# Kernel optimization log

Measured on AMD Instinct MI355X. Metric: run time of the kernel, lower is better.

Reference implementation:

```python
import jax, jax.numpy as jnp
import numpy as np

PROMPT_LEN = 2048
VOCAB = 49408
DIM = 768


def setup_inputs() -> dict:
    key = jax.random.key(0)
    k1, k2 = jax.random.split(key)
    # prompt_embs initialized ~ N(0, 0.02) per nn.init.normal_(std=0.02)
    prompt_embs = jax.random.normal(k1, (PROMPT_LEN, DIM), dtype=jnp.float32) * 0.02
    # codebook (CLIP embedding table), fixed data (not a trainable param)
    clip_embs = jax.random.normal(k2, (VOCAB, DIM), dtype=jnp.float32)
    return {"prompt_embs": prompt_embs, "clip_embs": clip_embs}


def _find_nearest(prompt_embs, clip_embs):
    # torch.cdist with p=2 -> Euclidean distance. argmin is invariant under sqrt,
    # so we use the expanded squared-distance form (single GEMM + norms),
    # avoiding materializing the [P, D]-broadcast difference tensor.
    p_sq = jnp.sum(prompt_embs * prompt_embs, axis=-1, keepdims=True)  # [P, 1]
    c_sq = jnp.sum(clip_embs * clip_embs, axis=-1)                      # [V]
    cross = jnp.einsum("pd,vd->pv", prompt_embs, clip_embs)            # [P, V]
    d2 = p_sq + c_sq[None, :] - 2.0 * cross                             # [P, V]
    return jnp.argmin(d2, axis=1)                                       # [P]


def reference(prompt_embs, clip_embs):
    prompt_ids = _find_nearest(prompt_embs, clip_embs)      # [P] int
    vocab_embs = clip_embs[prompt_ids, :]                   # [P, D] gather
    # straight-through: value = vocab_embs, gradient flows to prompt_embs
    out_embs = jax.lax.stop_gradient(vocab_embs - prompt_embs) + prompt_embs
    return out_embs, prompt_ids
```

## Files before the change

### kernel.cpp

```cpp
#include <hip/hip_runtime.h>
#include <float.h>

#define PROMPT_LEN 2048
#define VOCAB 49408
#define DIM 768
#define ROWS_TOTAL (VOCAB + PROMPT_LEN)
#define NS 32
#define BM 64
#define BN 64
#define KCH 128
#define NCHUNK (DIM / KCH)
#define LDK (KCH + 8)
#define CAND_MAX 4096
#define EPS 0.008f

typedef __attribute__((ext_vector_type(8))) short s8v;
typedef __attribute__((ext_vector_type(4))) float fx4;


__device__ inline unsigned short f2bf(float x) {
    unsigned u = __float_as_uint(x);
    u += 0x7FFFu + ((u >> 16) & 1u);
    return (unsigned short)(u >> 16);
}

__device__ inline void merge2(float& b1, float& b2, int& bi,
                              float y1, float y2, int yi) {
    if (y1 < b1) { b2 = fminf(b1, y2); b1 = y1; bi = yi; }
    else         { b2 = fminf(b2, fminf(y1, y2)); }
}

__global__ void __launch_bounds__(1024) k_sumsq(const float* __restrict__ prompt,
                                                const float* __restrict__ clip,
                                                float* __restrict__ csq,
                                                unsigned* __restrict__ scal) {
    int tid  = threadIdx.x;
    int wid  = tid >> 6;
    int lane = tid & 63;
    int base = blockIdx.x * 128 + wid * 8;

    if (blockIdx.x == 0 && tid == 0) scal[0] = 0u;

    float locMin = FLT_MAX, locMax = 0.f;
    for (int r = base; r < base + 8; r += 2) {
        const float* s0 = (r     < VOCAB) ? clip + (size_t)r * DIM
                                          : prompt + (size_t)(r - VOCAB) * DIM;
        const float* s1 = (r + 1 < VOCAB) ? clip + (size_t)(r + 1) * DIM
                                          : prompt + (size_t)(r + 1 - VOCAB) * DIM;
        float4 a0 = ((const float4*)s0)[lane];
        float4 a1 = ((const float4*)s0)[64 + lane];
        float4 a2 = ((const float4*)s0)[128 + lane];
        float4 b0 = ((const float4*)s1)[lane];
        float4 b1 = ((const float4*)s1)[64 + lane];
        float4 b2 = ((const float4*)s1)[128 + lane];
        float sA = a0.x*a0.x + a0.y*a0.y + a0.z*a0.z + a0.w*a0.w
                 + a1.x*a1.x + a1.y*a1.y + a1.z*a1.z + a1.w*a1.w
                 + a2.x*a2.x + a2.y*a2.y + a2.z*a2.z + a2.w*a2.w;
        float sB = b0.x*b0.x + b0.y*b0.y + b0.z*b0.z + b0.w*b0.w
                 + b1.x*b1.x + b1.y*b1.y + b1.z*b1.z + b1.w*b1.w
                 + b2.x*b2.x + b2.y*b2.y + b2.z*b2.z + b2.w*b2.w;
        #pragma unroll
        for (int m = 32; m >= 1; m >>= 1) {
            sA += __shfl_xor(sA, m, 64);
            sB += __shfl_xor(sB, m, 64);
        }
        if (r < VOCAB)     locMin = fminf(locMin, sA); else locMax = fmaxf(locMax, sA);
        if (r + 1 < VOCAB) locMin = fminf(locMin, sB); else locMax = fmaxf(locMax, sB);
        if (lane == 0) {
            if (r < VOCAB)     csq[r] = sA;
            if (r + 1 < VOCAB) csq[r + 1] = sB;
        }
    }
    __shared__ float smn[16], smx[16];
    if (lane == 0) { smn[wid] = locMin; smx[wid] = locMax; }
    __syncthreads();
    if (tid == 0) {
        float mn = FLT_MAX, mx = 0.f;
        #pragma unroll
        for (int w = 0; w < 16; ++w) { mn = fminf(mn, smn[w]); mx = fmaxf(mx, smx[w]); }
        atomicMin(&scal[1], __float_as_uint(mn));
        atomicMax((int*)&scal[2], (int)__float_as_uint(mx));
    }
}

__global__ void __launch_bounds__(256) k_compact(const float* __restrict__ csq,
                                                 int* __restrict__ cand,
                                                 unsigned* __restrict__ scal) {
    float cmin    = __uint_as_float(scal[1]);
    float pmax_sq = __uint_as_float(scal[2]);
    float B  = sqrtf(pmax_sq) * 1.0001f + 1e-6f;
    float U  = cmin + 2.f * B * sqrtf(cmin) + 1.0f;
    float sT = B + sqrtf(B * B + U);
    float T  = sT * sT;
    int v = blockIdx.x * 256 + threadIdx.x;
    if (v == 0) scal[3] = 0u;
    __shared__ int cnt, basep;
    if (threadIdx.x == 0) cnt = 0;
    __syncthreads();
    int keep = (v < VOCAB) && (csq[v] <= T);
    int pos = 0;
    if (keep) pos = atomicAdd(&cnt, 1);
    __syncthreads();
    if (threadIdx.x == 0 && cnt > 0) basep = atomicAdd((int*)&scal[0], cnt);
    __syncthreads();
    if (keep) cand[basep + pos] = v;
}

__global__ void __launch_bounds__(256) k_convert(const float* __restrict__ prompt,
                                                 const float* __restrict__ clip,
                                                 const int* __restrict__ cand,
                                                 const unsigned* __restrict__ scal,
                                                 unsigned short* __restrict__ PbH,
                                                 unsigned short* __restrict__ PbL,
                                                 unsigned short* __restrict__ CbH,
                                                 unsigned short* __restrict__ CbL) {
    int count = (int)scal[0];
    if (count > CAND_MAX) count = CAND_MAX;
    int rows = PROMPT_LEN + count;
    int wid  = threadIdx.x >> 6;
    int lane = threadIdx.x & 63;
    for (int r = blockIdx.x * 4 + wid; r < rows; r += gridDim.x * 4) {
        const float* src;
        unsigned short *dH, *dL;
        if (r < PROMPT_LEN) {
            src = prompt + (size_t)r * DIM;
            dH = PbH + (size_t)r * DIM;  dL = PbL + (size_t)r * DIM;
        } else {
            int i = r - PROMPT_LEN;
            src = clip + (size_t)cand[i] * DIM;
            dH = CbH + (size_t)i * DIM;  dL = CbL + (size_t)i * DIM;
        }
        #pragma unroll
        for (int i = 0; i < 3; ++i) {
            float4 x = ((const float4*)src)[i * 64 + lane];
            ushort4 h, l;
            h.x = f2bf(x.x); l.x = f2bf(x.x - __uint_as_float((unsigned)h.x << 16));
            h.y = f2bf(x.y); l.y = f2bf(x.y - __uint_as_float((unsigned)h.y << 16));
            h.z = f2bf(x.z); l.z = f2bf(x.z - __uint_as_float((unsigned)h.z << 16));
            h.w = f2bf(x.w); l.w = f2bf(x.w - __uint_as_float((unsigned)h.w << 16));
            ((ushort4*)dH)[i * 64 + lane] = h;
            ((ushort4*)dL)[i * 64 + lane] = l;
        }
    }
}

__global__ void __launch_bounds__(256, 2)
k_score(const unsigned short* __restrict__ PbH, const unsigned short* __restrict__ PbL,
        const unsigned short* __restrict__ CbH, const unsigned short* __restrict__ CbL,
        const float* __restrict__ csq, const int* __restrict__ cand,
        const unsigned* __restrict__ scal,
        float* __restrict__ AB1, float* __restrict__ AB2, int* __restrict__ AIdx) {
    int mi = blockIdx.x & 31;
    int s  = blockIdx.x >> 5;
    int m0 = mi * BM;
    int count = (int)scal[0];
    if (count > CAND_MAX) count = CAND_MAX;
    int ntiles = (count + BN - 1) / BN;

    int tid  = threadIdx.x;
    int lane = tid & 63;
    int wid  = tid >> 6;
    int wr32 = (wid >> 1) * 32;
    int wc32 = (wid & 1) * 32;
    int l15  = lane & 15;
    int l4   = lane >> 4;

    __shared__ unsigned short Ah[BM][LDK], Al[BM][LDK];
    __shared__ unsigned short Bh[BN][LDK], Bl[BN][LDK];
    __shared__ int   candS[BN];
    __shared__ float csqS[BN];
    __shared__ float mB1[BM][2], mB2[BM][2];
    __shared__ int   mBI[BM][2];

    int srow[4], scol[4], offA[4];
    #pragma unroll
    for (int f = 0; f < 4; ++f) {
        int j = tid + 256 * f;
        srow[f] = j >> 4;
        scol[f] = (j & 15) * 8;
        offA[f] = (m0 + srow[f]) * DIM + scol[f];
    }

    float rb1[2][4], rb2[2][4]; int rbi[2][4];
    #pragma unroll
    for (int fm = 0; fm < 2; ++fm)
        #pragma unroll
        for (int j = 0; j < 4; ++j) { rb1[fm][j] = FLT_MAX; rb2[fm][j] = FLT_MAX; rbi[fm][j] = 0x7fffffff; }

    for (int tile = s; tile < ntiles; tile += NS) {
        __syncthreads();
        if (tid < BN) {
            int ci = tile * BN + tid;
            int v  = (ci < count) ? cand[ci] : 0;
            candS[tid] = v;
            csqS[tid]  = (ci < count) ? csq[v] : FLT_MAX;
        }

        int offB[4];
        #pragma unroll
        for (int f = 0; f < 4; ++f) {
            int rowc = tile * BN + srow[f];
            if (rowc >= count) rowc = 0;
            offB[f] = rowc * DIM + scol[f];
        }

        fx4 acc00 = {0.f,0.f,0.f,0.f}, acc01 = {0.f,0.f,0.f,0.f};
        fx4 acc10 = {0.f,0.f,0.f,0.f}, acc11 = {0.f,0.f,0.f,0.f};

        s8v rAh[4], rAl[4], rBh[4], rBl[4];
        #pragma unroll
        for (int f = 0; f < 4; ++f) {
            rAh[f] = *(const s8v*)(PbH + offA[f]);
            rAl[f] = *(const s8v*)(PbL + offA[f]);
            rBh[f] = *(const s8v*)(CbH + offB[f]);
            rBl[f] = *(const s8v*)(CbL + offB[f]);
        }

        #pragma unroll
        for (int kc = 0; kc < NCHUNK; ++kc) {
            __syncthreads();
            #pragma unroll
            for (int f = 0; f < 4; ++f) {
                *(s8v*)&Ah[srow[f]][scol[f]] = rAh[f];
                *(s8v*)&Al[srow[f]][scol[f]] = rAl[f];
                *(s8v*)&Bh[srow[f]][scol[f]] = rBh[f];
                *(s8v*)&Bl[srow[f]][scol[f]] = rBl[f];
            }
            __syncthreads();
            if (kc + 1 < NCHUNK) {
                int off = (kc + 1) * KCH;
                #pragma unroll
                for (int f = 0; f < 4; ++f) {
                    rAh[f] = *(const s8v*)(PbH + offA[f] + off);
                    rAl[f] = *(const s8v*)(PbL + offA[f] + off);
                    rBh[f] = *(const s8v*)(CbH + offB[f] + off);
                    rBl[f] = *(const s8v*)(CbL + offB[f] + off);
                }
            }
            #pragma unroll
            for (int kk = 0; kk < KCH / 32; ++kk) {
                int ko = kk * 32 + l4 * 8;
                s8v ah0 = *(const s8v*)&Ah[wr32      + l15][ko];
                s8v ah1 = *(const s8v*)&Ah[wr32 + 16 + l15][ko];
                s8v al0 = *(const s8v*)&Al[wr32      + l15][ko];
                s8v al1 = *(const s8v*)&Al[wr32 + 16 + l15][ko];
                s8v bh0 = *(const s8v*)&Bh[wc32      + l15][ko];
                s8v bh1 = *(const s8v*)&Bh[wc32 + 16 + l15][ko];
                s8v bl0 = *(const s8v*)&Bl[wc32      + l15][ko];
                s8v bl1 = *(const s8v*)&Bl[wc32 + 16 + l15][ko];
                acc00 = __builtin_amdgcn_mfma_f32_16x16x32_bf16(ah0, bh0, acc00, 0, 0, 0);
                acc01 = __builtin_amdgcn_mfma_f32_16x16x32_bf16(ah0, bh1, acc01, 0, 0, 0);
                acc10 = __builtin_amdgcn_mfma_f32_16x16x32_bf16(ah1, bh0, acc10, 0, 0, 0);
                acc11 = __builtin_amdgcn_mfma_f32_16x16x32_bf16(ah1, bh1, acc11, 0, 0, 0);
                acc00 = __builtin_amdgcn_mfma_f32_16x16x32_bf16(al0, bh0, acc00, 0, 0, 0);
                acc01 = __builtin_amdgcn_mfma_f32_16x16x32_bf16(al0, bh1, acc01, 0, 0, 0);
                acc10 = __builtin_amdgcn_mfma_f32_16x16x32_bf16(al1, bh0, acc10, 0, 0, 0);
                acc11 = __builtin_amdgcn_mfma_f32_16x16x32_bf16(al1, bh1, acc11, 0, 0, 0);
                acc00 = __builtin_amdgcn_mfma_f32_16x16x32_bf16(ah0, bl0, acc00, 0, 0, 0);
                acc01 = __builtin_amdgcn_mfma_f32_16x16x32_bf16(ah0, bl1, acc01, 0, 0, 0);
                acc10 = __builtin_amdgcn_mfma_f32_16x16x32_bf16(ah1, bl0, acc10, 0, 0, 0);
                acc11 = __builtin_amdgcn_mfma_f32_16x16x32_bf16(ah1, bl1, acc11, 0, 0, 0);
            }
        }

        float cs0 = csqS[wc32 + l15];       int v0 = candS[wc32 + l15];
        float cs1 = csqS[wc32 + 16 + l15];  int v1 = candS[wc32 + 16 + l15];
        #pragma unroll
        for (int j = 0; j < 4; ++j) {
            if (cs0 < FLT_MAX) {
                float d2 = fmaf(-2.f, acc00[j], cs0);
                if (d2 < rb1[0][j]) { rb2[0][j] = rb1[0][j]; rb1[0][j] = d2; rbi[0][j] = v0; }
                else if (d2 <= rb2[0][j]) rb2[0][j] = d2;
                d2 = fmaf(-2.f, acc10[j], cs0);
                if (d2 < rb1[1][j]) { rb2[1][j] = rb1[1][j]; rb1[1][j] = d2; rbi[1][j] = v0; }
                else if (d2 <= rb2[1][j]) rb2[1][j] = d2;
            }
            if (cs1 < FLT_MAX) {
                float d2 = fmaf(-2.f, acc01[j], cs1);
                if (d2 < rb1[0][j]) { rb2[0][j] = rb1[0][j]; rb1[0][j] = d2; rbi[0][j] = v1; }
                else if (d2 <= rb2[0][j]) rb2[0][j] = d2;
                d2 = fmaf(-2.f, acc11[j], cs1);
                if (d2 < rb1[1][j]) { rb2[1][j] = rb1[1][j]; rb1[1][j] = d2; rbi[1][j] = v1; }
                else if (d2 <= rb2[1][j]) rb2[1][j] = d2;
            }
        }
    }

    #pragma unroll
    for (int fm = 0; fm < 2; ++fm)
        #pragma unroll
        for (int j = 0; j < 4; ++j) {
            float b1 = rb1[fm][j], b2 = rb2[fm][j]; int bi = rbi[fm][j];
            #pragma unroll
            for (int msk = 1; msk <= 8; msk <<= 1) {
                float y1 = __shfl_xor(b1, msk, 64);
                float y2 = __shfl_xor(b2, msk, 64);
                int   yi = __shfl_xor(bi, msk, 64);
                merge2(b1, b2, bi, y1, y2, yi);
            }
            if (l15 == 0) {
                int rl = wr32 + fm * 16 + l4 * 4 + j;
                int wc = (wid & 1);
                mB1[rl][wc] = b1; mB2[rl][wc] = b2; mBI[rl][wc] = bi;
            }
        }
    __syncthreads();
    if (tid < BM) {
        float B1 = mB1[tid][0], B2 = mB2[tid][0]; int BI = mBI[tid][0];
        merge2(B1, B2, BI, mB1[tid][1], mB2[tid][1], mBI[tid][1]);
        int m = m0 + tid;
        AB1[m * NS + s]  = B1;
        AB2[m * NS + s]  = B2;
        AIdx[m * NS + s] = BI;
    }
}

__global__ void __launch_bounds__(256) k_merge(const float* __restrict__ prompt,
                                               const float* __restrict__ clip,
                                               const float* __restrict__ AB1,
                                               const float* __restrict__ AB2,
                                               const int* __restrict__ AIdx,
                                               unsigned* __restrict__ scal,
                                               int* __restrict__ amb,
                                               float* __restrict__ out) {
    int wid  = threadIdx.x >> 6;
    int lane = threadIdx.x & 63;
    int m = blockIdx.x * 4 + wid;
    int s = lane & 31;
    int count = (int)scal[0];

    float b1 = AB1[m * NS + s];
    float b2 = AB2[m * NS + s];
    int   bi = AIdx[m * NS + s];
    #pragma unroll
    for (int msk = 1; msk <= 16; msk <<= 1) {
        float y1 = __shfl_xor(b1, msk, 64);
        float y2 = __shfl_xor(b2, msk, 64);
        int   yi = __shfl_xor(bi, msk, 64);
        merge2(b1, b2, bi, y1, y2, yi);
    }

    if (count > CAND_MAX || b2 - b1 < EPS) {
        if (lane == 0) {
            int pos = atomicAdd((int*)&scal[3], 1);
            amb[pos] = m;
        }
    } else {
        const float* crow = clip + (size_t)bi * DIM;
        const float* prow = prompt + (size_t)m * DIM;
        #pragma unroll
        for (int i = 0; i < 3; ++i) {
            float4 c = ((const float4*)crow)[i * 64 + lane];
            float4 p = ((const float4*)prow)[i * 64 + lane];
            float4 o;
            o.x = (c.x - p.x) + p.x;
            o.y = (c.y - p.y) + p.y;
            o.z = (c.z - p.z) + p.z;
            o.w = (c.w - p.w) + p.w;
            ((float4*)(out + (size_t)m * DIM))[i * 64 + lane] = o;
        }
        if (lane == 0) out[(size_t)PROMPT_LEN * DIM + m] = (float)bi;
    }
}

__global__ void __launch_bounds__(1024) k_fallback(const float* __restrict__ prompt,
                                                   const float* __restrict__ clip,
                                                   const int* __restrict__ cand,
                                                   const unsigned* __restrict__ scal,
                                                   const int* __restrict__ amb,
                                                   float* __restrict__ out) {
    int nAmb  = (int)scal[3];
    int count = (int)scal[0];
    int tid  = threadIdx.x;
    int wid  = tid >> 6;
    int lane = tid & 63;

    __shared__ double fB[16];
    __shared__ int    fI[16];
    __shared__ int    sWin;

    for (int a = blockIdx.x; a < nAmb; a += gridDim.x) {
        int m = amb[a];
        const float* prow = prompt + (size_t)m * DIM;
        double pd[12];
        #pragma unroll
        for (int i = 0; i < 3; ++i) {
            float4 v = ((const float4*)prow)[i * 64 + lane];
            pd[i*4+0] = (double)v.x; pd[i*4+1] = (double)v.y;
            pd[i*4+2] = (double)v.z; pd[i*4+3] = (double)v.w;
        }
        double best = 1e300;
        int bestIdx = 0x7fffffff;
        for (int ci = wid; ci < count; ci += 16) {
            int v = cand[ci];
            const float* crow = clip + (size_t)v * DIM;
            double sd = 0.0;
            #pragma unroll
            for (int i = 0; i < 3; ++i) {
                float4 c = ((const float4*)crow)[i * 64 + lane];
                double d0 = (double)c.x - pd[i*4+0];
                double d1 = (double)c.y - pd[i*4+1];
                double d2 = (double)c.z - pd[i*4+2];
                double d3 = (double)c.w - pd[i*4+3];
                sd = fma(d0, d0, sd); sd = fma(d1, d1, sd);
                sd = fma(d2, d2, sd); sd = fma(d3, d3, sd);
            }
            #pragma unroll
            for (int msk = 32; msk >= 1; msk >>= 1) sd += __shfl_xor(sd, msk, 64);
            if (sd < best || (sd == best && v < bestIdx)) { best = sd; bestIdx = v; }
        }
        if (lane == 0) { fB[wid] = best; fI[wid] = bestIdx; }
        __syncthreads();
        if (tid == 0) {
            double b = fB[0]; int bi2 = fI[0];
            #pragma unroll
            for (int w = 1; w < 16; ++w)
                if (fB[w] < b || (fB[w] == b && fI[w] < bi2)) { b = fB[w]; bi2 = fI[w]; }
            sWin = bi2;
        }
        __syncthreads();
        int win = sWin;

        if (tid < 192) {
            float4 c = ((const float4*)(clip + (size_t)win * DIM))[tid];
            float4 p = ((const float4*)prow)[tid];
            float4 o;
            o.x = (c.x - p.x) + p.x;
            o.y = (c.y - p.y) + p.y;
            o.z = (c.z - p.z) + p.z;
            o.w = (c.w - p.w) + p.w;
            ((float4*)(out + (size_t)m * DIM))[tid] = o;
        }
        if (tid == 0) out[(size_t)PROMPT_LEN * DIM + m] = (float)win;
        __syncthreads();
    }
}

extern "C" void kernel_launch(void* const* d_in, const int* in_sizes, int n_in,
                              void* d_out, int out_size, void* d_ws, size_t ws_size,
                              hipStream_t stream) {
    const float* prompt = (const float*)d_in[0];
    const float* clip   = (const float*)d_in[1];
    float* out = (float*)d_out;

    char* w = (char*)d_ws;
    float*    csq  = (float*)w;                    w += (size_t)VOCAB * 4;
    int*      cand = (int*)w;                      w += (size_t)VOCAB * 4;
    unsigned* scal = (unsigned*)w;                 w += 32;
    float*    AB1  = (float*)w;                    w += (size_t)PROMPT_LEN * NS * 4;
    float*    AB2  = (float*)w;                    w += (size_t)PROMPT_LEN * NS * 4;
    int*      AIdx = (int*)w;                      w += (size_t)PROMPT_LEN * NS * 4;
    int*      amb  = (int*)w;                      w += (size_t)PROMPT_LEN * 4;
    unsigned short* PbH = (unsigned short*)w;      w += (size_t)PROMPT_LEN * DIM * 2;
    unsigned short* PbL = (unsigned short*)w;      w += (size_t)PROMPT_LEN * DIM * 2;
    unsigned short* CbH = (unsigned short*)w;      w += (size_t)CAND_MAX * DIM * 2;
    unsigned short* CbL = (unsigned short*)w;      w += (size_t)CAND_MAX * DIM * 2;

    k_sumsq<<<ROWS_TOTAL / 128, 1024, 0, stream>>>(prompt, clip, csq, scal);
    k_compact<<<(VOCAB + 255) / 256, 256, 0, stream>>>(csq, cand, scal);
    k_convert<<<1024, 256, 0, stream>>>(prompt, clip, cand, scal, PbH, PbL, CbH, CbL);
    k_score<<<32 * NS, 256, 0, stream>>>(PbH, PbL, CbH, CbL, csq, cand, scal,
                                         AB1, AB2, AIdx);
    k_merge<<<PROMPT_LEN / 4, 256, 0, stream>>>(prompt, clip, AB1, AB2, AIdx, scal, amb, out);
    k_fallback<<<128, 1024, 0, stream>>>(prompt, clip, cand, scal, amb, out);
}
```

Before: 307.8 us.

## Fuse compact with convert and merge into score via last-block reduction

Merges the candidate-compaction and bf16 split conversion into a single kernel, folds the per-row argmin merge and output write into the score kernel using an atomic counter so the last split block per row tile does the reduction, and cuts the K-split count from 32 to 8. It also caches candidate norms contiguously and uses smaller sumsq blocks. The goal is to remove two launches and the intermediate round trips. In exchange it adds atomic and fence synchronisation, and because each score block now handles more tiles there may be less parallelism in the GEMM stage.

```diff
diff --git a/kernel.cpp b/kernel.cpp
--- a/kernel.cpp
+++ b/kernel.cpp
@@ -5,7 +5,8 @@
 #define VOCAB 49408
 #define DIM 768
 #define ROWS_TOTAL (VOCAB + PROMPT_LEN)
-#define NS 32
+#define NS 8
+#define NMI (PROMPT_LEN / 64)
 #define BM 64
 #define BN 64
 #define KCH 128
@@ -30,14 +31,30 @@
     else         { b2 = fminf(b2, fminf(y1, y2)); }
 }
 
-__global__ void __launch_bounds__(1024) k_sumsq(const float* __restrict__ prompt,
-                                                const float* __restrict__ clip,
-                                                float* __restrict__ csq,
-                                                unsigned* __restrict__ scal) {
+__device__ inline void conv_row(const float* __restrict__ src,
+                                unsigned short* __restrict__ dH,
+                                unsigned short* __restrict__ dL, int lane) {
+    #pragma unroll
+    for (int i = 0; i < 3; ++i) {
+        float4 x = ((const float4*)src)[i * 64 + lane];
+        ushort4 h, l;
+        h.x = f2bf(x.x); l.x = f2bf(x.x - __uint_as_float((unsigned)h.x << 16));
+        h.y = f2bf(x.y); l.y = f2bf(x.y - __uint_as_float((unsigned)h.y << 16));
+        h.z = f2bf(x.z); l.z = f2bf(x.z - __uint_as_float((unsigned)h.z << 16));
+        h.w = f2bf(x.w); l.w = f2bf(x.w - __uint_as_float((unsigned)h.w << 16));
+        ((ushort4*)dH)[i * 64 + lane] = h;
+        ((ushort4*)dL)[i * 64 + lane] = l;
+    }
+}
+
+__global__ void __launch_bounds__(256) k_sumsq(const float* __restrict__ prompt,
+                                               const float* __restrict__ clip,
+                                               float* __restrict__ csq,
+                                               unsigned* __restrict__ scal) {
     int tid  = threadIdx.x;
     int wid  = tid >> 6;
     int lane = tid & 63;
-    int base = blockIdx.x * 128 + wid * 8;
+    int base = blockIdx.x * 32 + wid * 8;
 
     if (blockIdx.x == 0 && tid == 0) scal[0] = 0u;
 
@@ -71,90 +88,87 @@
             if (r + 1 < VOCAB) csq[r + 1] = sB;
         }
     }
-    __shared__ float smn[16], smx[16];
+    __shared__ float smn[4], smx[4];
     if (lane == 0) { smn[wid] = locMin; smx[wid] = locMax; }
     __syncthreads();
     if (tid == 0) {
         float mn = FLT_MAX, mx = 0.f;
         #pragma unroll
-        for (int w = 0; w < 16; ++w) { mn = fminf(mn, smn[w]); mx = fmaxf(mx, smx[w]); }
+        for (int w = 0; w < 4; ++w) { mn = fminf(mn, smn[w]); mx = fmaxf(mx, smx[w]); }
         atomicMin(&scal[1], __float_as_uint(mn));
         atomicMax((int*)&scal[2], (int)__float_as_uint(mx));
     }
 }
 
-__global__ void __launch_bounds__(256) k_compact(const float* __restrict__ csq,
-                                                 int* __restrict__ cand,
-                                                 unsigned* __restrict__ scal) {
+__global__ void __launch_bounds__(256) k_compact_convert(
+        const float* __restrict__ prompt, const float* __restrict__ clip,
+        const float* __restrict__ csq,
+        int* __restrict__ cand, float* __restrict__ candCsq,
+        unsigned* __restrict__ scal, int* __restrict__ cnt,
+        unsigned short* __restrict__ PbH, unsigned short* __restrict__ PbL,
+        unsigned short* __restrict__ CbH, unsigned short* __restrict__ CbL) {
     float cmin    = __uint_as_float(scal[1]);
     float pmax_sq = __uint_as_float(scal[2]);
     float B  = sqrtf(pmax_sq) * 1.0001f + 1e-6f;
     float U  = cmin + 2.f * B * sqrtf(cmin) + 1.0f;
     float sT = B + sqrtf(B * B + U);
     float T  = sT * sT;
-    int v = blockIdx.x * 256 + threadIdx.x;
-    if (v == 0) scal[3] = 0u;
-    __shared__ int cnt, basep;
-    if (threadIdx.x == 0) cnt = 0;
-    __syncthreads();
-    int keep = (v < VOCAB) && (csq[v] <= T);
+
+    int tid = threadIdx.x;
+    int v   = blockIdx.x * 256 + tid;
+    if (blockIdx.x == 0) {
+        if (tid == 0) scal[3] = 0u;
+        if (tid < NMI) cnt[tid] = 0;
+    }
+    __shared__ int cntS, basep;
+    __shared__ int kvS[256];
+    if (tid == 0) cntS = 0;
+    __syncthreads();
+    float cs = csq[v];
+    int keep = (cs <= T);
     int pos = 0;
-    if (keep) pos = atomicAdd(&cnt, 1);
-    __syncthreads();
-    if (threadIdx.x == 0 && cnt > 0) basep = atomicAdd((int*)&scal[0], cnt);
-    __syncthreads();
-    if (keep) cand[basep + pos] = v;
-}
-
-__global__ void __launch_bounds__(256) k_convert(const float* __restrict__ prompt,
-                                                 const float* __restrict__ clip,
-                                                 const int* __restrict__ cand,
-                                                 const unsigned* __restrict__ scal,
-                                                 unsigned short* __restrict__ PbH,
-                                                 unsigned short* __restrict__ PbL,
-                                                 unsigned short* __restrict__ CbH,
-                                                 unsigned short* __restrict__ CbL) {
-    int count = (int)scal[0];
-    if (count > CAND_MAX) count = CAND_MAX;
-    int rows = PROMPT_LEN + count;
-    int wid  = threadIdx.x >> 6;
-    int lane = threadIdx.x & 63;
-    for (int r = blockIdx.x * 4 + wid; r < rows; r += gridDim.x * 4) {
-        const float* src;
-        unsigned short *dH, *dL;
-        if (r < PROMPT_LEN) {
-            src = prompt + (size_t)r * DIM;
-            dH = PbH + (size_t)r * DIM;  dL = PbL + (size_t)r * DIM;
-        } else {
-            int i = r - PROMPT_LEN;
-            src = clip + (size_t)cand[i] * DIM;
-            dH = CbH + (size_t)i * DIM;  dL = CbL + (size_t)i * DIM;
-        }
-        #pragma unroll
-        for (int i = 0; i < 3; ++i) {
-            float4 x = ((const float4*)src)[i * 64 + lane];
-            ushort4 h, l;
-            h.x = f2bf(x.x); l.x = f2bf(x.x - __uint_as_float((unsigned)h.x << 16));
-            h.y = f2bf(x.y); l.y = f2bf(x.y - __uint_as_float((unsigned)h.y << 16));
-            h.z = f2bf(x.z); l.z = f2bf(x.z - __uint_as_float((unsigned)h.z << 16));
-            h.w = f2bf(x.w); l.w = f2bf(x.w - __uint_as_float((unsigned)h.w << 16));
-            ((ushort4*)dH)[i * 64 + lane] = h;
-            ((ushort4*)dL)[i * 64 + lane] = l;
-        }
+    if (keep) pos = atomicAdd(&cntS, 1);
+    __syncthreads();
+    if (tid == 0 && cntS > 0) basep = atomicAdd((int*)&scal[0], cntS);
+    __syncthreads();
+    if (keep) {
+        cand[basep + pos]    = v;
+        candCsq[basep + pos] = cs;
+        kvS[pos] = v;
+    }
+    __syncthreads();
+
+    int nk   = cntS;
+    int wid  = tid >> 6;
+    int lane = tid & 63;
+    for (int i = wid; i < nk; i += 4) {
+        int dst = basep + i;
+        if (dst >= CAND_MAX) break;
+        conv_row(clip + (size_t)kvS[i] * DIM,
+                 CbH + (size_t)dst * DIM, CbL + (size_t)dst * DIM, lane);
+    }
+    #pragma unroll
+    for (int j = wid; j < 11; j += 4) {
+        int r = blockIdx.x + 193 * j;
+        if (r < PROMPT_LEN)
+            conv_row(prompt + (size_t)r * DIM,
+                     PbH + (size_t)r * DIM, PbL + (size_t)r * DIM, lane);
     }
 }
 
 __global__ void __launch_bounds__(256, 2)
 k_score(const unsigned short* __restrict__ PbH, const unsigned short* __restrict__ PbL,
         const unsigned short* __restrict__ CbH, const unsigned short* __restrict__ CbL,
-        const float* __restrict__ csq, const int* __restrict__ cand,
-        const unsigned* __restrict__ scal,
-        float* __restrict__ AB1, float* __restrict__ AB2, int* __restrict__ AIdx) {
-    int mi = blockIdx.x & 31;
+        const float* __restrict__ candCsq, const int* __restrict__ cand,
+        unsigned* __restrict__ scal, int* __restrict__ cnt,
+        float* __restrict__ AB1, float* __restrict__ AB2, int* __restrict__ AIdx,
+        const float* __restrict__ prompt, const float* __restrict__ clip,
+        int* __restrict__ amb, float* __restrict__ out) {
+    int mi = blockIdx.x & (NMI - 1);
     int s  = blockIdx.x >> 5;
     int m0 = mi * BM;
-    int count = (int)scal[0];
-    if (count > CAND_MAX) count = CAND_MAX;
+    int rawCount = (int)scal[0];
+    int count = rawCount > CAND_MAX ? CAND_MAX : rawCount;
     int ntiles = (count + BN - 1) / BN;
 
     int tid  = threadIdx.x;
@@ -169,8 +183,10 @@
     __shared__ unsigned short Bh[BN][LDK], Bl[BN][LDK];
     __shared__ int   candS[BN];
     __shared__ float csqS[BN];
-    __shared__ float mB1[BM][2], mB2[BM][2];
-    __shared__ int   mBI[BM][2];
+    __shared__ float mB1[BM][4], mB2[BM][4];
+    __shared__ int   mBI[BM][4];
+    __shared__ int   winS[BM], clearS[BM];
+    __shared__ int   lastS;
 
     int srow[4], scol[4], offA[4];
     #pragma unroll
@@ -191,9 +207,8 @@
         __syncthreads();
         if (tid < BN) {
             int ci = tile * BN + tid;
-            int v  = (ci < count) ? cand[ci] : 0;
-            candS[tid] = v;
-            csqS[tid]  = (ci < count) ? csq[v] : FLT_MAX;
+            candS[tid] = (ci < count) ? cand[ci] : 0;
+            csqS[tid]  = (ci < count) ? candCsq[ci] : FLT_MAX;
         }
 
         int offB[4];
@@ -300,8 +315,7 @@
             }
             if (l15 == 0) {
                 int rl = wr32 + fm * 16 + l4 * 4 + j;
-                int wc = (wid & 1);
-                mB1[rl][wc] = b1; mB2[rl][wc] = b2; mBI[rl][wc] = bi;
+                mB1[rl][wid & 1] = b1; mB2[rl][wid & 1] = b2; mBI[rl][wid & 1] = bi;
             }
         }
     __syncthreads();
@@ -309,45 +323,53 @@
         float B1 = mB1[tid][0], B2 = mB2[tid][0]; int BI = mBI[tid][0];
         merge2(B1, B2, BI, mB1[tid][1], mB2[tid][1], mBI[tid][1]);
         int m = m0 + tid;
-        AB1[m * NS + s]  = B1;
-        AB2[m * NS + s]  = B2;
-        AIdx[m * NS + s] = BI;
-    }
-}
-
-__global__ void __launch_bounds__(256) k_merge(const float* __restrict__ prompt,
-                                               const float* __restrict__ clip,
-                                               const float* __restrict__ AB1,
-                                               const float* __restrict__ AB2,
-                                               const int* __restrict__ AIdx,
-                                               unsigned* __restrict__ scal,
-                                               int* __restrict__ amb,
-                                               float* __restrict__ out) {
-    int wid  = threadIdx.x >> 6;
-    int lane = threadIdx.x & 63;
-    int m = blockIdx.x * 4 + wid;
-    int s = lane & 31;
-    int count = (int)scal[0];
-
-    float b1 = AB1[m * NS + s];
-    float b2 = AB2[m * NS + s];
-    int   bi = AIdx[m * NS + s];
-    #pragma unroll
-    for (int msk = 1; msk <= 16; msk <<= 1) {
-        float y1 = __shfl_xor(b1, msk, 64);
-        float y2 = __shfl_xor(b2, msk, 64);
-        int   yi = __shfl_xor(bi, msk, 64);
-        merge2(b1, b2, bi, y1, y2, yi);
-    }
-
-    if (count > CAND_MAX || b2 - b1 < EPS) {
-        if (lane == 0) {
+        __hip_atomic_store(&AB1[m * NS + s], B1, __ATOMIC_RELAXED, __HIP_MEMORY_SCOPE_AGENT);
+        __hip_atomic_store(&AB2[m * NS + s], B2, __ATOMIC_RELAXED, __HIP_MEMORY_SCOPE_AGENT);
+        __hip_atomic_store(&AIdx[m * NS + s], BI, __ATOMIC_RELAXED, __HIP_MEMORY_SCOPE_AGENT);
+    }
+    __syncthreads();
+    if (tid == 0) {
+        __threadfence();
+        int old = atomicAdd(&cnt[mi], 1);
+        lastS = (old == NS - 1);
+    }
+    __syncthreads();
+    if (!lastS) return;
+    __threadfence();
+
+    {
+        int r = tid & 63, g = tid >> 6;
+        int m = m0 + r;
+        float b1 = FLT_MAX, b2 = FLT_MAX; int bi = 0x7fffffff;
+        #pragma unroll
+        for (int ss = 0; ss < 2; ++ss) {
+            int s2 = g * 2 + ss;
+            float y1 = __hip_atomic_load(&AB1[m * NS + s2], __ATOMIC_RELAXED, __HIP_MEMORY_SCOPE_AGENT);
+            float y2 = __hip_atomic_load(&AB2[m * NS + s2], __ATOMIC_RELAXED, __HIP_MEMORY_SCOPE_AGENT);
+            int   yi = __hip_atomic_load(&AIdx[m * NS + s2], __ATOMIC_RELAXED, __HIP_MEMORY_SCOPE_AGENT);
+            merge2(b1, b2, bi, y1, y2, yi);
+        }
+        mB1[r][g] = b1; mB2[r][g] = b2; mBI[r][g] = bi;
+    }
+    __syncthreads();
+    if (tid < BM) {
+        float B1 = mB1[tid][0], B2 = mB2[tid][0]; int BI = mBI[tid][0];
+        #pragma unroll
+        for (int gg = 1; gg < 4; ++gg)
+            merge2(B1, B2, BI, mB1[tid][gg], mB2[tid][gg], mBI[tid][gg]);
+        int clear = (rawCount <= CAND_MAX) && (B2 - B1 >= EPS);
+        winS[tid] = BI; clearS[tid] = clear;
+        if (!clear) {
             int pos = atomicAdd((int*)&scal[3], 1);
-            amb[pos] = m;
-        }
-    } else {
-        const float* crow = clip + (size_t)bi * DIM;
-        const float* prow = prompt + (size_t)m * DIM;
+            amb[pos] = m0 + tid;
+        }
+    }
+    __syncthreads();
+    for (int rr = wid; rr < BM; rr += 4) {
+        if (!clearS[rr]) continue;
+        int mm = m0 + rr, win = winS[rr];
+        const float* crow = clip + (size_t)win * DIM;
+        const float* prow = prompt + (size_t)mm * DIM;
         #pragma unroll
         for (int i = 0; i < 3; ++i) {
             float4 c = ((const float4*)crow)[i * 64 + lane];
@@ -357,9 +379,9 @@
             o.y = (c.y - p.y) + p.y;
             o.z = (c.z - p.z) + p.z;
             o.w = (c.w - p.w) + p.w;
-            ((float4*)(out + (size_t)m * DIM))[i * 64 + lane] = o;
-        }
-        if (lane == 0) out[(size_t)PROMPT_LEN * DIM + m] = (float)bi;
+            ((float4*)(out + (size_t)mm * DIM))[i * 64 + lane] = o;
+        }
+        if (lane == 0) out[(size_t)PROMPT_LEN * DIM + mm] = (float)win;
     }
 }
 
@@ -444,23 +466,24 @@
     float* out = (float*)d_out;
 
     char* w = (char*)d_ws;
-    float*    csq  = (float*)w;                    w += (size_t)VOCAB * 4;
-    int*      cand = (int*)w;                      w += (size_t)VOCAB * 4;
-    unsigned* scal = (unsigned*)w;                 w += 32;
-    float*    AB1  = (float*)w;                    w += (size_t)PROMPT_LEN * NS * 4;
-    float*    AB2  = (float*)w;                    w += (size_t)PROMPT_LEN * NS * 4;
-    int*      AIdx = (int*)w;                      w += (size_t)PROMPT_LEN * NS * 4;
-    int*      amb  = (int*)w;                      w += (size_t)PROMPT_LEN * 4;
+    float*    csq     = (float*)w;                 w += (size_t)VOCAB * 4;
+    int*      cand    = (int*)w;                   w += (size_t)VOCAB * 4;
+    float*    candCsq = (float*)w;                 w += (size_t)VOCAB * 4;
+    unsigned* scal    = (unsigned*)w;              w += 32;
+    float*    AB1     = (float*)w;                 w += (size_t)PROMPT_LEN * NS * 4;
+    float*    AB2     = (float*)w;                 w += (size_t)PROMPT_LEN * NS * 4;
+    int*      AIdx    = (int*)w;                   w += (size_t)PROMPT_LEN * NS * 4;
+    int*      amb     = (int*)w;                   w += (size_t)PROMPT_LEN * 4;
+    int*      cnt     = (int*)w;                   w += 128;
     unsigned short* PbH = (unsigned short*)w;      w += (size_t)PROMPT_LEN * DIM * 2;
     unsigned short* PbL = (unsigned short*)w;      w += (size_t)PROMPT_LEN * DIM * 2;
     unsigned short* CbH = (unsigned short*)w;      w += (size_t)CAND_MAX * DIM * 2;
     unsigned short* CbL = (unsigned short*)w;      w += (size_t)CAND_MAX * DIM * 2;
 
-    k_sumsq<<<ROWS_TOTAL / 128, 1024, 0, stream>>>(prompt, clip, csq, scal);
-    k_compact<<<(VOCAB + 255) / 256, 256, 0, stream>>>(csq, cand, scal);
-    k_convert<<<1024, 256, 0, stream>>>(prompt, clip, cand, scal, PbH, PbL, CbH, CbL);
-    k_score<<<32 * NS, 256, 0, stream>>>(PbH, PbL, CbH, CbL, csq, cand, scal,
-                                         AB1, AB2, AIdx);
-    k_merge<<<PROMPT_LEN / 4, 256, 0, stream>>>(prompt, clip, AB1, AB2, AIdx, scal, amb, out);
+    k_sumsq<<<ROWS_TOTAL / 32, 256, 0, stream>>>(prompt, clip, csq, scal);
+    k_compact_convert<<<VOCAB / 256, 256, 0, stream>>>(prompt, clip, csq, cand, candCsq,
+                                                       scal, cnt, PbH, PbL, CbH, CbL);
+    k_score<<<NMI * NS, 256, 0, stream>>>(PbH, PbL, CbH, CbL, candCsq, cand, scal, cnt,
+                                          AB1, AB2, AIdx, prompt, clip, amb, out);
     k_fallback<<<128, 1024, 0, stream>>>(prompt, clip, cand, scal, amb, out);
 }
```

New measurement: 332.8 us. +8.1%, slower.

## Fuse candidate compaction with bf16 conversion and shrink sumsq grid

Applied to the files above, without the earlier changes.

Merges the compaction and bf16 hi/lo conversion kernels into one. Each block compacts its slice of vocab rows and converts its kept candidate rows, while also converting four prompt rows. This removes one launch and the separate pass that re-read the candidate list. It also stores candidate squared norms contiguously so the scoring kernel avoids an indirect csq lookup, and it changes the sumsq kernel to a grid-stride loop over 512 blocks. The block-local conversion puts a different amount of work on each block, so load balance depends on how candidates are distributed.

```diff
diff --git a/kernel.cpp b/kernel.cpp
--- a/kernel.cpp
+++ b/kernel.cpp
@@ -24,6 +24,22 @@
     return (unsigned short)(u >> 16);
 }
 
+__device__ inline void conv_row(const float* __restrict__ src,
+                                unsigned short* __restrict__ dH,
+                                unsigned short* __restrict__ dL, int lane) {
+    #pragma unroll
+    for (int i = 0; i < 3; ++i) {
+        float4 x = ((const float4*)src)[i * 64 + lane];
+        ushort4 h, l;
+        h.x = f2bf(x.x); l.x = f2bf(x.x - __uint_as_float((unsigned)h.x << 16));
+        h.y = f2bf(x.y); l.y = f2bf(x.y - __uint_as_float((unsigned)h.y << 16));
+        h.z = f2bf(x.z); l.z = f2bf(x.z - __uint_as_float((unsigned)h.z << 16));
+        h.w = f2bf(x.w); l.w = f2bf(x.w - __uint_as_float((unsigned)h.w << 16));
+        ((ushort4*)dH)[i * 64 + lane] = h;
+        ((ushort4*)dL)[i * 64 + lane] = l;
+    }
+}
+
 __device__ inline void merge2(float& b1, float& b2, int& bi,
                               float y1, float y2, int yi) {
     if (y1 < b1) { b2 = fminf(b1, y2); b1 = y1; bi = yi; }
@@ -37,14 +53,15 @@
     int tid  = threadIdx.x;
     int wid  = tid >> 6;
     int lane = tid & 63;
-    int base = blockIdx.x * 128 + wid * 8;
+    int gw   = blockIdx.x * 16 + wid;
 
     if (blockIdx.x == 0 && tid == 0) scal[0] = 0u;
 
     float locMin = FLT_MAX, locMax = 0.f;
-    for (int r = base; r < base + 8; r += 2) {
-        const float* s0 = (r     < VOCAB) ? clip + (size_t)r * DIM
-                                          : prompt + (size_t)(r - VOCAB) * DIM;
+    for (int p = gw; p < ROWS_TOTAL / 2; p += 8192) {
+        int r = 2 * p;
+        const float* s0 = (r < VOCAB) ? clip + (size_t)r * DIM
+                                      : prompt + (size_t)(r - VOCAB) * DIM;
         const float* s1 = (r + 1 < VOCAB) ? clip + (size_t)(r + 1) * DIM
                                           : prompt + (size_t)(r + 1 - VOCAB) * DIM;
         float4 a0 = ((const float4*)s0)[lane];
@@ -83,71 +100,68 @@
     }
 }
 
-__global__ void __launch_bounds__(256) k_compact(const float* __restrict__ csq,
-                                                 int* __restrict__ cand,
-                                                 unsigned* __restrict__ scal) {
+__global__ void __launch_bounds__(256) k_compact_convert(
+        const float* __restrict__ prompt, const float* __restrict__ clip,
+        const float* __restrict__ csq,
+        int* __restrict__ cand, float* __restrict__ candCsq,
+        unsigned* __restrict__ scal,
+        unsigned short* __restrict__ PbH, unsigned short* __restrict__ PbL,
+        unsigned short* __restrict__ CbH, unsigned short* __restrict__ CbL) {
+    int tid  = threadIdx.x;
+    int wid  = tid >> 6;
+    int lane = tid & 63;
+    int bx   = blockIdx.x;
+
+    if (bx == 0 && tid == 0) scal[3] = 0u;
+
+    {
+        int r = bx * 4 + wid;
+        conv_row(prompt + (size_t)r * DIM,
+                 PbH + (size_t)r * DIM, PbL + (size_t)r * DIM, lane);
+    }
+
+    if (bx >= VOCAB / 256) return;
+
     float cmin    = __uint_as_float(scal[1]);
     float pmax_sq = __uint_as_float(scal[2]);
     float B  = sqrtf(pmax_sq) * 1.0001f + 1e-6f;
     float U  = cmin + 2.f * B * sqrtf(cmin) + 1.0f;
     float sT = B + sqrtf(B * B + U);
     float T  = sT * sT;
-    int v = blockIdx.x * 256 + threadIdx.x;
-    if (v == 0) scal[3] = 0u;
-    __shared__ int cnt, basep;
-    if (threadIdx.x == 0) cnt = 0;
-    __syncthreads();
-    int keep = (v < VOCAB) && (csq[v] <= T);
+
+    int v = bx * 256 + tid;
+    __shared__ int cntS, basep;
+    __shared__ int kvS[256];
+    if (tid == 0) cntS = 0;
+    __syncthreads();
+    float cs = csq[v];
+    int keep = (cs <= T);
     int pos = 0;
-    if (keep) pos = atomicAdd(&cnt, 1);
-    __syncthreads();
-    if (threadIdx.x == 0 && cnt > 0) basep = atomicAdd((int*)&scal[0], cnt);
-    __syncthreads();
-    if (keep) cand[basep + pos] = v;
-}
-
-__global__ void __launch_bounds__(256) k_convert(const float* __restrict__ prompt,
-                                                 const float* __restrict__ clip,
-                                                 const int* __restrict__ cand,
-                                                 const unsigned* __restrict__ scal,
-                                                 unsigned short* __restrict__ PbH,
-                                                 unsigned short* __restrict__ PbL,
-                                                 unsigned short* __restrict__ CbH,
-                                                 unsigned short* __restrict__ CbL) {
-    int count = (int)scal[0];
-    if (count > CAND_MAX) count = CAND_MAX;
-    int rows = PROMPT_LEN + count;
-    int wid  = threadIdx.x >> 6;
-    int lane = threadIdx.x & 63;
-    for (int r = blockIdx.x * 4 + wid; r < rows; r += gridDim.x * 4) {
-        const float* src;
-        unsigned short *dH, *dL;
-        if (r < PROMPT_LEN) {
-            src = prompt + (size_t)r * DIM;
-            dH = PbH + (size_t)r * DIM;  dL = PbL + (size_t)r * DIM;
-        } else {
-            int i = r - PROMPT_LEN;
-            src = clip + (size_t)cand[i] * DIM;
-            dH = CbH + (size_t)i * DIM;  dL = CbL + (size_t)i * DIM;
-        }
-        #pragma unroll
-        for (int i = 0; i < 3; ++i) {
-            float4 x = ((const float4*)src)[i * 64 + lane];
-            ushort4 h, l;
-            h.x = f2bf(x.x); l.x = f2bf(x.x - __uint_as_float((unsigned)h.x << 16));
-            h.y = f2bf(x.y); l.y = f2bf(x.y - __uint_as_float((unsigned)h.y << 16));
-            h.z = f2bf(x.z); l.z = f2bf(x.z - __uint_as_float((unsigned)h.z << 16));
-            h.w = f2bf(x.w); l.w = f2bf(x.w - __uint_as_float((unsigned)h.w << 16));
-            ((ushort4*)dH)[i * 64 + lane] = h;
-            ((ushort4*)dL)[i * 64 + lane] = l;
-        }
+    if (keep) pos = atomicAdd(&cntS, 1);
+    __syncthreads();
+    if (tid == 0 && cntS > 0) basep = atomicAdd((int*)&scal[0], cntS);
+    __syncthreads();
+    if (keep) {
+        int dst = basep + pos;
+        cand[dst]    = v;
+        candCsq[dst] = cs;
+        kvS[pos] = v;
+    }
+    __syncthreads();
+
+    int nk = cntS;
+    for (int i = wid; i < nk; i += 4) {
+        int dst = basep + i;
+        if (dst >= CAND_MAX) break;
+        conv_row(clip + (size_t)kvS[i] * DIM,
+                 CbH + (size_t)dst * DIM, CbL + (size_t)dst * DIM, lane);
     }
 }
 
 __global__ void __launch_bounds__(256, 2)
 k_score(const unsigned short* __restrict__ PbH, const unsigned short* __restrict__ PbL,
         const unsigned short* __restrict__ CbH, const unsigned short* __restrict__ CbL,
-        const float* __restrict__ csq, const int* __restrict__ cand,
+        const float* __restrict__ candCsq, const int* __restrict__ cand,
         const unsigned* __restrict__ scal,
         float* __restrict__ AB1, float* __restrict__ AB2, int* __restrict__ AIdx) {
     int mi = blockIdx.x & 31;
@@ -191,9 +205,8 @@
         __syncthreads();
         if (tid < BN) {
             int ci = tile * BN + tid;
-            int v  = (ci < count) ? cand[ci] : 0;
-            candS[tid] = v;
-            csqS[tid]  = (ci < count) ? csq[v] : FLT_MAX;
+            candS[tid] = (ci < count) ? cand[ci] : 0;
+            csqS[tid]  = (ci < count) ? candCsq[ci] : FLT_MAX;
         }
 
         int offB[4];
@@ -300,8 +313,7 @@
             }
             if (l15 == 0) {
                 int rl = wr32 + fm * 16 + l4 * 4 + j;
-                int wc = (wid & 1);
-                mB1[rl][wc] = b1; mB2[rl][wc] = b2; mBI[rl][wc] = bi;
+                mB1[rl][wid & 1] = b1; mB2[rl][wid & 1] = b2; mBI[rl][wid & 1] = bi;
             }
         }
     __syncthreads();
@@ -444,22 +456,23 @@
     float* out = (float*)d_out;
 
     char* w = (char*)d_ws;
-    float*    csq  = (float*)w;                    w += (size_t)VOCAB * 4;
-    int*      cand = (int*)w;                      w += (size_t)VOCAB * 4;
-    unsigned* scal = (unsigned*)w;                 w += 32;
-    float*    AB1  = (float*)w;                    w += (size_t)PROMPT_LEN * NS * 4;
-    float*    AB2  = (float*)w;                    w += (size_t)PROMPT_LEN * NS * 4;
-    int*      AIdx = (int*)w;                      w += (size_t)PROMPT_LEN * NS * 4;
-    int*      amb  = (int*)w;                      w += (size_t)PROMPT_LEN * 4;
+    float*    csq     = (float*)w;                 w += (size_t)VOCAB * 4;
+    int*      cand    = (int*)w;                   w += (size_t)VOCAB * 4;
+    float*    candCsq = (float*)w;                 w += (size_t)VOCAB * 4;
+    unsigned* scal    = (unsigned*)w;              w += 32;
+    float*    AB1     = (float*)w;                 w += (size_t)PROMPT_LEN * NS * 4;
+    float*    AB2     = (float*)w;                 w += (size_t)PROMPT_LEN * NS * 4;
+    int*      AIdx    = (int*)w;                   w += (size_t)PROMPT_LEN * NS * 4;
+    int*      amb     = (int*)w;                   w += (size_t)PROMPT_LEN * 4;
     unsigned short* PbH = (unsigned short*)w;      w += (size_t)PROMPT_LEN * DIM * 2;
     unsigned short* PbL = (unsigned short*)w;      w += (size_t)PROMPT_LEN * DIM * 2;
     unsigned short* CbH = (unsigned short*)w;      w += (size_t)CAND_MAX * DIM * 2;
     unsigned short* CbL = (unsigned short*)w;      w += (size_t)CAND_MAX * DIM * 2;
 
-    k_sumsq<<<ROWS_TOTAL / 128, 1024, 0, stream>>>(prompt, clip, csq, scal);
-    k_compact<<<(VOCAB + 255) / 256, 256, 0, stream>>>(csq, cand, scal);
-    k_convert<<<1024, 256, 0, stream>>>(prompt, clip, cand, scal, PbH, PbL, CbH, CbL);
-    k_score<<<32 * NS, 256, 0, stream>>>(PbH, PbL, CbH, CbL, csq, cand, scal,
+    k_sumsq<<<512, 1024, 0, stream>>>(prompt, clip, csq, scal);
+    k_compact_convert<<<512, 256, 0, stream>>>(prompt, clip, csq, cand, candCsq,
+                                               scal, PbH, PbL, CbH, CbL);
+    k_score<<<32 * NS, 256, 0, stream>>>(PbH, PbL, CbH, CbL, candCsq, cand, scal,
                                          AB1, AB2, AIdx);
     k_merge<<<PROMPT_LEN / 4, 256, 0, stream>>>(prompt, clip, AB1, AB2, AIdx, scal, amb, out);
     k_fallback<<<128, 1024, 0, stream>>>(prompt, clip, cand, scal, amb, out);
```

Result: no change. 306.2 us (-0.5%).
